# Kernel optimization log

Hardware: AMD Instinct MI355X
Metric: run time of the kernel (lower is better)

## Reference

```python
import jax, jax.numpy as jnp
import numpy as np

N, E, IN_DIM, HID, HEADS, LAT = 50000, 800000, 128, 32, 4, 32


def _gat_params(key, fin, heads, cout):
    k1, k2, k3 = jax.random.split(key, 3)
    s = 1.0 / np.sqrt(fin)
    W = jax.random.uniform(k1, (fin, heads * cout), minval=-s, maxval=s, dtype=jnp.float32)
    a_src = jax.random.normal(k2, (heads, cout), dtype=jnp.float32) * 0.1
    a_dst = jax.random.normal(k3, (heads, cout), dtype=jnp.float32) * 0.1
    b = jnp.zeros((heads * cout,), dtype=jnp.float32)
    return W, a_src, a_dst, b


def setup_inputs() -> dict:
    key = jax.random.key(0)
    ks = jax.random.split(key, 8)
    x = jax.random.normal(ks[0], (N, IN_DIM), dtype=jnp.float32)
    edge_index = jax.random.randint(ks[1], (2, E), 0, N, dtype=jnp.int64)
    W1, a1s, a1d, b1 = _gat_params(ks[2], IN_DIM, HEADS, HID)
    W2, a2s, a2d, b2 = _gat_params(ks[3], HID * HEADS, HEADS, HID)
    Wl, als, ald, bl = _gat_params(ks[4], HID * HEADS, 1, LAT)
    Wd, ads_, add_, bd = _gat_params(ks[5], LAT, 1, HID)
    sdec = 1.0 / np.sqrt(HID)
    Wdec = jax.random.uniform(ks[6], (HID, IN_DIM), minval=-sdec, maxval=sdec, dtype=jnp.float32)
    bdec = jnp.zeros((IN_DIM,), dtype=jnp.float32)
    return {"x": x, "edge_index": edge_index,
            "W1": W1, "a1s": a1s, "a1d": a1d, "b1": b1,
            "W2": W2, "a2s": a2s, "a2d": a2d, "b2": b2,
            "Wl": Wl, "als": als, "ald": ald, "bl": bl,
            "Wd": Wd, "ads": ads_, "add": add_, "bd": bd,
            "Wdec": Wdec, "bdec": bdec}


def gat_conv(x, src, dst, W, a_s, a_d, b, n, concat=True):
    """PyG-style GATConv (eval mode, self-loops already in src/dst)."""
    H, C = a_s.shape
    h = (x @ W).reshape(n, H, C)                      # [N,H,C]
    alpha_src = jnp.sum(h * a_s, axis=-1)             # [N,H]
    alpha_dst = jnp.sum(h * a_d, axis=-1)             # [N,H]
    e = jax.nn.leaky_relu(alpha_src[src] + alpha_dst[dst], 0.2)  # [E,H]
    m = jax.ops.segment_max(e, dst, num_segments=n)
    m = jnp.where(jnp.isfinite(m), m, 0.0)
    ex = jnp.exp(e - m[dst])
    denom = jax.ops.segment_sum(ex, dst, num_segments=n)
    coef = ex / (denom[dst] + 1e-16)                  # [E,H]
    out = jax.ops.segment_sum(coef[:, :, None] * h[src], dst, num_segments=n)  # [N,H,C]
    out = out.reshape(n, H * C) if concat else out.mean(axis=1)
    return out + b


def reference(x, edge_index, W1, a1s, a1d, b1, W2, a2s, a2d, b2,
              Wl, als, ald, bl, Wd, ads, add, bd, Wdec, bdec):
    n = x.shape[0]
    # add self-loops (PyG GATConv default)
    loops = jnp.arange(n, dtype=edge_index.dtype)
    src = jnp.concatenate([edge_index[0], loops])
    dst = jnp.concatenate([edge_index[1], loops])
    lrelu = lambda v: jax.nn.leaky_relu(v, 0.01)
    x1 = lrelu(gat_conv(x, src, dst, W1, a1s, a1d, b1, n))
    x2 = lrelu(gat_conv(x1, src, dst, W2, a2s, a2d, b2, n))
    z = gat_conv(x2, src, dst, Wl, als, ald, bl, n)
    xr = lrelu(gat_conv(z, src, dst, Wd, ads, add, bd, n))
    reconstructed = xr @ Wdec + bdec + x
    return reconstructed, z
```

## Files before the change

### kernel.cpp

```cpp
#include <hip/hip_runtime.h>
#include <math.h>

#define CAP 64

typedef __attribute__((ext_vector_type(8))) short short8;
typedef __attribute__((ext_vector_type(4))) float f32x4;

__device__ __forceinline__ float lrelu02(float v) { return v > 0.f ? v : 0.2f * v; }
__device__ __forceinline__ float lrelu01(float v) { return v > 0.f ? v : 0.01f * v; }

__device__ __forceinline__ float bfl(unsigned u) { return __uint_as_float(u << 16); }
__device__ __forceinline__ float bfh(unsigned u) { return __uint_as_float(u & 0xffff0000u); }
__device__ __forceinline__ unsigned short f2bf(float f) {
  unsigned u = __float_as_uint(f);
  return (unsigned short)((u + 0x7fffu + ((u >> 16) & 1u)) >> 16);
}
__device__ __forceinline__ unsigned pk2bf(float lo, float hi) {
  return (unsigned)f2bf(lo) | ((unsigned)f2bf(hi) << 16);
}

__global__ __launch_bounds__(256) void prep_k(const int* __restrict__ ei, int* __restrict__ deg,
                                              unsigned short* __restrict__ cols, int E, int nr, int Nn,
                                              const float* __restrict__ W1, const float* __restrict__ W2,
                                              const float* __restrict__ Wl,
                                              unsigned short* __restrict__ t1, unsigned short* __restrict__ t2,
                                              unsigned short* __restrict__ tl) {
  if (blockIdx.x < 2048) {
    const int r = blockIdx.x & 7;
    const int c = blockIdx.x >> 3;
    const unsigned lo = (unsigned)(r * nr);
    const unsigned hi = (unsigned)min(Nn, (r + 1) * nr);
    const int chunk = (E + 255) >> 8;
    const int e0 = c * chunk;
    const int e1 = min(E, e0 + chunk);
    for (int e = e0 + (int)threadIdx.x; e < e1; e += 256) {
      unsigned d = (unsigned)ei[E + e];
      if (d >= lo && d < hi) {
        int s = ei[e];
        int pos = atomicAdd(&deg[d], 1);
        if (pos < CAP) cols[(size_t)d * CAP + pos] = (unsigned short)s;
      }
    }
  } else {
    int b = blockIdx.x - 2048, tid = threadIdx.x;
    const float* src; unsigned short* dst; int K, NC, base;
    if (b < 64)       { src = W1; dst = t1; K = 128; NC = 128; base = 0; }
    else if (b < 128) { src = W2; dst = t2; K = 128; NC = 128; base = 64; }
    else              { src = Wl; dst = tl; K = 128; NC = 32;  base = 128; }
    int e = (b - base) * 256 + tid;
    if (e < K * NC) {
      int k = e / NC, c2 = e - k * NC;
      dst[c2 * K + k] = f2bf(src[e]);
    }
  }
}

template<int K, int NC, bool ALPHA, bool IN32>
__global__ __launch_bounds__(256) void gemm_mfma(const void* __restrict__ Av,
                                                 const unsigned short* __restrict__ Wt,
                                                 unsigned short* __restrict__ Cb,
                                                 const float* __restrict__ a_s, const float* __restrict__ a_d,
                                                 float* __restrict__ asrc, float* __restrict__ adst, int M) {
  constexpr int BM = (NC == 128) ? 64 : 128;
  constexpr int NKS = K / 32;
  constexpr int RS = (NC == 128) ? 4 : 2;
  constexpr int SWZ = 7;
  constexpr int CH = BM * K / 2048;
  __shared__ unsigned short At[BM * K];
  const int tid = threadIdx.x;
  const int wid = tid >> 6, lane = tid & 63;
  const int g = lane >> 4, l15 = lane & 15;
  const int row0 = blockIdx.x * BM;

  short8 wf[NKS][2];
  const int cglob0 = ((NC == 128) ? 32 * wid : 0) + l15;
#pragma unroll
  for (int ks = 0; ks < NKS; ++ks)
#pragma unroll
    for (int cf = 0; cf < 2; ++cf)
      wf[ks][cf] = *(const short8*)(Wt + (size_t)(cglob0 + 16 * cf) * K + ks * 32 + g * 8);

  uint4 ra[CH];
  if constexpr (IN32) {
    const float* Af = (const float*)Av;
#pragma unroll
    for (int c = 0; c < CH; ++c) {
      int ch = c * 256 + tid;
      int row = ch * 8 / K;
      int col = ch * 8 - row * K;
      float4 lo = {0.f, 0.f, 0.f, 0.f}, hi = {0.f, 0.f, 0.f, 0.f};
      if (row0 + row < M) {
        lo = *(const float4*)(Af + (size_t)(row0 + row) * K + col);
        hi = *(const float4*)(Af + (size_t)(row0 + row) * K + col + 4);
      }
      ra[c] = make_uint4(pk2bf(lo.x, lo.y), pk2bf(lo.z, lo.w), pk2bf(hi.x, hi.y), pk2bf(hi.z, hi.w));
    }
  } else {
    const unsigned short* Ab = (const unsigned short*)Av;
#pragma unroll
    for (int c = 0; c < CH; ++c) {
      int ch = c * 256 + tid;
      int row = ch * 8 / K;
      ra[c] = (row0 + row < M) ? *(const uint4*)(Ab + (size_t)row0 * K + ch * 8)
                               : make_uint4(0u, 0u, 0u, 0u);
    }
  }
#pragma unroll
  for (int c = 0; c < CH; ++c) {
    int ch = c * 256 + tid;
    int row = ch * 8 / K;
    int off = ch * 16 - row * (2 * K);
    *(uint4*)((char*)At + row * (2 * K) + (off ^ ((row & SWZ) << 4))) = ra[c];
  }
  __syncthreads();

  f32x4 acc[RS][2];
#pragma unroll
  for (int r = 0; r < RS; ++r)
#pragma unroll
    for (int cf = 0; cf < 2; ++cf) acc[r][cf] = (f32x4){0.f, 0.f, 0.f, 0.f};

  const int rwave = (NC == 128) ? 0 : 32 * wid;
#pragma unroll
  for (int ks = 0; ks < NKS; ++ks) {
#pragma unroll
    for (int r = 0; r < RS; ++r) {
      int row = rwave + 16 * r + l15;
      int off = ks * 64 + g * 16;
      short8 af = *(const short8*)((const char*)At + row * (2 * K) + (off ^ ((row & SWZ) << 4)));
#pragma unroll
      for (int cf = 0; cf < 2; ++cf)
        acc[r][cf] = __builtin_amdgcn_mfma_f32_16x16x32_bf16(wf[ks][cf], af, acc[r][cf], 0, 0, 0);
    }
  }

#pragma unroll
  for (int r = 0; r < RS; ++r) {
    const int row = row0 + rwave + 16 * r + l15;
    const bool ok = row < M;
#pragma unroll
    for (int cf = 0; cf < 2; ++cf) {
      const int colbase = ((NC == 128) ? 32 * wid : 0) + 16 * cf + 4 * g;
      if (ok) {
        ushort4 o;
        o.x = f2bf(acc[r][cf][0]); o.y = f2bf(acc[r][cf][1]);
        o.z = f2bf(acc[r][cf][2]); o.w = f2bf(acc[r][cf][3]);
        *(ushort4*)(Cb + (size_t)row * NC + colbase) = o;
      }
    }
    if constexpr (ALPHA) {
      constexpr int H = NC / 32;
      const int head = (NC == 128) ? wid : 0;
      float ps = 0.f, pd = 0.f;
#pragma unroll
      for (int cf = 0; cf < 2; ++cf) {
        float4 sa = *(const float4*)(a_s + head * 32 + 16 * cf + 4 * g);
        float4 da = *(const float4*)(a_d + head * 32 + 16 * cf + 4 * g);
        ps += acc[r][cf][0] * sa.x + acc[r][cf][1] * sa.y + acc[r][cf][2] * sa.z + acc[r][cf][3] * sa.w;
        pd += acc[r][cf][0] * da.x + acc[r][cf][1] * da.y + acc[r][cf][2] * da.z + acc[r][cf][3] * da.w;
      }
      ps += __shfl_xor(ps, 16, 64); pd += __shfl_xor(pd, 16, 64);
      ps += __shfl_xor(ps, 32, 64); pd += __shfl_xor(pd, 32, 64);
      if (g == 0 && ok) {
        asrc[(size_t)row * H + head] = ps;
        adst[(size_t)row * H + head] = pd;
      }
    }
  }
}

template<int ACT>
__global__ __launch_bounds__(256) void agg128_k(const unsigned short* __restrict__ Hb,
                                                const float* __restrict__ asrc,
                                                const float* __restrict__ adst,
                                                const int* __restrict__ deg,
                                                const unsigned short* __restrict__ cols,
                                                const float* __restrict__ bias,
                                                unsigned short* __restrict__ Y, int Nn) {
  __shared__ float wl[4][256];
  __shared__ int sl[4][64];
  const int wid = threadIdx.x >> 6, lane = threadIdx.x & 63;
  const int node = blockIdx.x * 4 + wid;
  if (node >= Nn) return;
  const int eidx = lane >> 2, h4 = lane & 3;
  const float adr = adst[node * 4 + h4];
  const float asr = asrc[node * 4 + h4];
  int cnt = deg[node];
  cnt = cnt > CAP ? CAP : cnt;
  const unsigned short* __restrict__ cl = cols + (size_t)node * CAP;
  float dn = 0.f;
  for (int c0 = 0; c0 < cnt; c0 += 16) {
    int e = c0 + eidx;
    bool valid = e < cnt;
    int s = valid ? (int)cl[e] : 0;
    float w = valid ? __expf(lrelu02(asrc[s * 4 + h4] + adr)) : 0.f;
    wl[wid][e * 4 + h4] = w;
    if (h4 == 0) sl[wid][e] = s * 16;
    dn += w;
  }
  dn += __shfl_xor(dn, 4, 64);
  dn += __shfl_xor(dn, 8, 64);
  dn += __shfl_xor(dn, 16, 64);
  dn += __shfl_xor(dn, 32, 64);
  float wself = __expf(lrelu02(asr + adr));
  dn += wself;
  float inv = 1.f / (dn + 1e-16f);
  float wsinv = wself * inv;
  for (int j = lane; j < cnt * 4; j += 64) wl[wid][j] *= inv;
  float wns = __shfl(wsinv, (lane & 15) >> 2, 64);
  __builtin_amdgcn_wave_barrier();

  const uint4* __restrict__ HB = (const uint4*)Hb;
  const int sub = lane >> 4;
  const int c8 = lane & 15;
  const int h = c8 >> 2;
  float a0 = 0.f, a1 = 0.f, a2 = 0.f, a3 = 0.f, a4 = 0.f, a5 = 0.f, a6 = 0.f, a7 = 0.f;
  float p0 = 0.f, p1 = 0.f, p2 = 0.f, p3 = 0.f, p4 = 0.f, p5 = 0.f, p6 = 0.f, p7 = 0.f;
  int i = sub;
  for (; i + 4 < cnt; i += 8) {
    int o0 = sl[wid][i];
    int o1 = sl[wid][i + 4];
    float w0 = wl[wid][i * 4 + h];
    float w1 = wl[wid][(i + 4) * 4 + h];
    uint4 u0 = HB[o0 + c8];
    uint4 u1 = HB[o1 + c8];
    a0 += w0 * bfl(u0.x); a1 += w0 * bfh(u0.x); a2 += w0 * bfl(u0.y); a3 += w0 * bfh(u0.y);
    a4 += w0 * bfl(u0.z); a5 += w0 * bfh(u0.z); a6 += w0 * bfl(u0.w); a7 += w0 * bfh(u0.w);
    p0 += w1 * bfl(u1.x); p1 += w1 * bfh(u1.x); p2 += w1 * bfl(u1.y); p3 += w1 * bfh(u1.y);
    p4 += w1 * bfl(u1.z); p5 += w1 * bfh(u1.z); p6 += w1 * bfl(u1.w); p7 += w1 * bfh(u1.w);
  }
  for (; i < cnt; i += 4) {
    int o0 = sl[wid][i];
    float w0 = wl[wid][i * 4 + h];
    uint4 u0 = HB[o0 + c8];
    a0 += w0 * bfl(u0.x); a1 += w0 * bfh(u0.x); a2 += w0 * bfl(u0.y); a3 += w0 * bfh(u0.y);
    a4 += w0 * bfl(u0.z); a5 += w0 * bfh(u0.z); a6 += w0 * bfl(u0.w); a7 += w0 * bfh(u0.w);
  }
  a0 += p0; a1 += p1; a2 += p2; a3 += p3; a4 += p4; a5 += p5; a6 += p6; a7 += p7;
#pragma unroll
  for (int off = 16; off <= 32; off <<= 1) {
    a0 += __shfl_xor(a0, off, 64); a1 += __shfl_xor(a1, off, 64);
    a2 += __shfl_xor(a2, off, 64); a3 += __shfl_xor(a3, off, 64);
    a4 += __shfl_xor(a4, off, 64); a5 += __shfl_xor(a5, off, 64);
    a6 += __shfl_xor(a6, off, 64); a7 += __shfl_xor(a7, off, 64);
  }
  if (lane < 16) {
    uint4 us = HB[node * 16 + c8];
    float4 b0 = *(const float4*)(bias + c8 * 8);
    float4 b1 = *(const float4*)(bias + c8 * 8 + 4);
    float o0 = a0 + wns * bfl(us.x) + b0.x;
    float o1 = a1 + wns * bfh(us.x) + b0.y;
    float o2 = a2 + wns * bfl(us.y) + b0.z;
    float o3 = a3 + wns * bfh(us.y) + b0.w;
    float o4 = a4 + wns * bfl(us.z) + b1.x;
    float o5 = a5 + wns * bfh(us.z) + b1.y;
    float o6 = a6 + wns * bfl(us.w) + b1.z;
    float o7 = a7 + wns * bfh(us.w) + b1.w;
    if (ACT == 1) {
      o0 = lrelu01(o0); o1 = lrelu01(o1); o2 = lrelu01(o2); o3 = lrelu01(o3);
      o4 = lrelu01(o4); o5 = lrelu01(o5); o6 = lrelu01(o6); o7 = lrelu01(o7);
    }
    ((uint4*)Y)[(size_t)node * 16 + c8] =
        make_uint4(pk2bf(o0, o1), pk2bf(o2, o3), pk2bf(o4, o5), pk2bf(o6, o7));
  }
}

template<int ACT>
__device__ __forceinline__ float4 agg32_core(const unsigned short* __restrict__ Hb,
                                             const float* __restrict__ asrc, const float* __restrict__ adst,
                                             const int* __restrict__ deg,
                                             const unsigned short* __restrict__ cols,
                                             const float* __restrict__ bias,
                                             float (*wl)[64], int (*sl)[64],
                                             int wid, int lane, int node) {
  const float adr = adst[node], asr = asrc[node];
  int cnt = deg[node];
  cnt = cnt > CAP ? CAP : cnt;
  const unsigned short* __restrict__ cl = cols + (size_t)node * CAP;
  int s = (lane < cnt) ? (int)cl[lane] : 0;
  float w = (lane < cnt) ? __expf(lrelu02(asrc[s] + adr)) : 0.f;
  float dn = w;
#pragma unroll
  for (int off = 32; off >= 1; off >>= 1) dn += __shfl_xor(dn, off, 64);
  float ws = __expf(lrelu02(asr + adr));
  dn += ws;
  float inv = 1.f / (dn + 1e-16f);
  wl[wid][lane] = w * inv;
  sl[wid][lane] = s * 8;
  __builtin_amdgcn_wave_barrier();

  const uint2* __restrict__ HB = (const uint2*)Hb;
  const int sub = lane >> 3;
  const int c = lane & 7;
  float a0 = 0.f, a1 = 0.f, a2 = 0.f, a3 = 0.f;
  float p0 = 0.f, p1 = 0.f, p2 = 0.f, p3 = 0.f;
  int i = sub;
  for (; i + 8 < cnt; i += 16) {
    int o0 = sl[wid][i];
    int o1 = sl[wid][i + 8];
    float w0 = wl[wid][i];
    float w1 = wl[wid][i + 8];
    uint2 u0 = HB[o0 + c];
    uint2 u1 = HB[o1 + c];
    a0 += w0 * bfl(u0.x); a1 += w0 * bfh(u0.x); a2 += w0 * bfl(u0.y); a3 += w0 * bfh(u0.y);
    p0 += w1 * bfl(u1.x); p1 += w1 * bfh(u1.x); p2 += w1 * bfl(u1.y); p3 += w1 * bfh(u1.y);
  }
  for (; i < cnt; i += 8) {
    int o0 = sl[wid][i];
    float w0 = wl[wid][i];
    uint2 u0 = HB[o0 + c];
    a0 += w0 * bfl(u0.x); a1 += w0 * bfh(u0.x); a2 += w0 * bfl(u0.y); a3 += w0 * bfh(u0.y);
  }
  a0 += p0; a1 += p1; a2 += p2; a3 += p3;
#pragma unroll
  for (int off = 8; off <= 32; off <<= 1) {
    a0 += __shfl_xor(a0, off, 64); a1 += __shfl_xor(a1, off, 64);
    a2 += __shfl_xor(a2, off, 64); a3 += __shfl_xor(a3, off, 64);
  }
  float4 out = make_float4(0.f, 0.f, 0.f, 0.f);
  if (lane < 8) {
    uint2 us = HB[node * 8 + c];
    float wns = ws * inv;
    float4 bb = ((const float4*)bias)[c];
    out.x = a0 + wns * bfl(us.x) + bb.x;
    out.y = a1 + wns * bfh(us.x) + bb.y;
    out.z = a2 + wns * bfl(us.y) + bb.z;
    out.w = a3 + wns * bfh(us.y) + bb.w;
    if (ACT == 1) { out.x = lrelu01(out.x); out.y = lrelu01(out.y); out.z = lrelu01(out.z); out.w = lrelu01(out.w); }
  }
  return out;
}

__global__ __launch_bounds__(256) void agg32_l3_k(const unsigned short* __restrict__ Hb,
                                                  const float* __restrict__ asrc, const float* __restrict__ adst,
                                                  const int* __restrict__ deg,
                                                  const unsigned short* __restrict__ cols,
                                                  const float* __restrict__ bl,
                                                  const float* __restrict__ Wd,
                                                  const float* __restrict__ ads, const float* __restrict__ add_,
                                                  float* __restrict__ zout, unsigned short* __restrict__ H4,
                                                  float* __restrict__ asrcB, float* __restrict__ adstB, int Nn) {
  __shared__ float Wd_l[32 * 32];
  __shared__ float wl[4][64];
  __shared__ int sl[4][64];
  __shared__ float zb[4][32];
  {
    int t = threadIdx.x * 4;
    *(float4*)&Wd_l[t] = *(const float4*)(Wd + t);
  }
  __syncthreads();
  const int wid = threadIdx.x >> 6, lane = threadIdx.x & 63;
  const int node = blockIdx.x * 4 + wid;
  if (node >= Nn) return;

  float4 z = agg32_core<0>(Hb, asrc, adst, deg, cols, bl, wl, sl, wid, lane, node);
  const int c = lane & 7;
  if (lane < 8) {
    ((float4*)zout)[(size_t)node * 8 + c] = z;
    *(float4*)&zb[wid][c * 4] = z;
  }
  __builtin_amdgcn_wave_barrier();

  float h4 = 0.f;
  const int j = lane & 31;
#pragma unroll 8
  for (int k = 0; k < 32; ++k) h4 += zb[wid][k] * Wd_l[k * 32 + j];
  float ps = 0.f, pd = 0.f;
  if (lane < 32) {
    H4[(size_t)node * 32 + j] = f2bf(h4);
    ps = h4 * ads[j];
    pd = h4 * add_[j];
  }
#pragma unroll
  for (int off = 1; off <= 16; off <<= 1) { ps += __shfl_xor(ps, off, 64); pd += __shfl_xor(pd, off, 64); }
  if (lane == 0) {
    asrcB[node] = ps;
    adstB[node] = pd;
  }
}

__global__ __launch_bounds__(256) void agg32_l4_k(const unsigned short* __restrict__ Hb,
                                                  const float* __restrict__ asrc, const float* __restrict__ adst,
                                                  const int* __restrict__ deg,
                                                  const unsigned short* __restrict__ cols,
                                                  const float* __restrict__ bd,
                                                  const float* __restrict__ Wdec,
                                                  const float* __restrict__ bdec,
                                                  const float* __restrict__ x,
                                                  float* __restrict__ rec, int Nn) {
  __shared__ float Wdec_l[32 * 128];
  __shared__ float wl[4][64];
  __shared__ int sl[4][64];
  __shared__ float xb[4][32];
  {
    int t = threadIdx.x * 16;
#pragma unroll
    for (int q = 0; q < 4; ++q)
      *(float4*)&Wdec_l[t + q * 4] = *(const float4*)(Wdec + t + q * 4);
  }
  __syncthreads();
  const int wid = threadIdx.x >> 6, lane = threadIdx.x & 63;
  const int node = blockIdx.x * 4 + wid;
  if (node >= Nn) return;

  float4 xr = agg32_core<1>(Hb, asrc, adst, deg, cols, bd, wl, sl, wid, lane, node);
  const int c = lane & 7;
  if (lane < 8) *(float4*)&xb[wid][c * 4] = xr;
  __builtin_amdgcn_wave_barrier();

  float r0 = 0.f, r1 = 0.f;
#pragma unroll 8
  for (int k = 0; k < 32; ++k) {
    float xv = xb[wid][k];
    r0 += xv * Wdec_l[k * 128 + lane];
    r1 += xv * Wdec_l[k * 128 + lane + 64];
  }
  r0 += bdec[lane] + x[(size_t)node * 128 + lane];
  r1 += bdec[lane + 64] + x[(size_t)node * 128 + lane + 64];
  rec[(size_t)node * 128 + lane] = r0;
  rec[(size_t)node * 128 + lane + 64] = r1;
}

extern "C" void kernel_launch(void* const* d_in, const int* in_sizes, int n_in,
                              void* d_out, int out_size, void* d_ws, size_t ws_size,
                              hipStream_t stream) {
  const float* x = (const float*)d_in[0];
  const int* ei = (const int*)d_in[1];
  const float* W1 = (const float*)d_in[2];
  const float* a1s = (const float*)d_in[3];
  const float* a1d = (const float*)d_in[4];
  const float* b1 = (const float*)d_in[5];
  const float* W2 = (const float*)d_in[6];
  const float* a2s = (const float*)d_in[7];
  const float* a2d = (const float*)d_in[8];
  const float* b2 = (const float*)d_in[9];
  const float* Wl = (const float*)d_in[10];
  const float* als = (const float*)d_in[11];
  const float* ald = (const float*)d_in[12];
  const float* bl = (const float*)d_in[13];
  const float* Wd = (const float*)d_in[14];
  const float* ads = (const float*)d_in[15];
  const float* add_ = (const float*)d_in[16];
  const float* bd = (const float*)d_in[17];
  const float* Wdec = (const float*)d_in[18];
  const float* bdec = (const float*)d_in[19];

  const int N = in_sizes[0] / 128;
  const int E = in_sizes[1] / 2;
  const int nr = (N + 7) / 8;

  char* ws = (char*)d_ws;
  auto alloc = [&](size_t bytes) {
    char* p = ws;
    ws += (bytes + 255) & ~(size_t)255;
    return p;
  };
  unsigned short* cols = (unsigned short*)alloc((size_t)N * CAP * 2);
  int* deg = (int*)alloc((size_t)N * 4);
  unsigned short* hb16 = (unsigned short*)alloc((size_t)N * 128 * 2);
  float* asrc = (float*)alloc((size_t)N * 4 * 4);
  float* adst = (float*)alloc((size_t)N * 4 * 4);
  float* asrcB = (float*)alloc((size_t)N * 4);
  float* adstB = (float*)alloc((size_t)N * 4);
  unsigned short* x12 = (unsigned short*)alloc((size_t)N * 128 * 2);
  unsigned short* hb2 = (unsigned short*)alloc((size_t)N * 32 * 2);
  unsigned short* W1t = (unsigned short*)alloc(128 * 128 * 2);
  unsigned short* W2t = (unsigned short*)alloc(128 * 128 * 2);
  unsigned short* Wlt = (unsigned short*)alloc(128 * 32 * 2);

  float* rec = (float*)d_out;
  float* zout = (float*)d_out + (size_t)N * 128;

  hipMemsetAsync(deg, 0, (size_t)N * 4, stream);
  prep_k<<<2192, 256, 0, stream>>>(ei, deg, cols, E, nr, N, W1, W2, Wl, W1t, W2t, Wlt);

  const int gG128 = (N + 63) / 64;
  const int gG32 = (N + 127) / 128;
  const int gAg = (N + 3) / 4;

  gemm_mfma<128, 128, true, true><<<gG128, 256, 0, stream>>>(
      x, W1t, hb16, a1s, a1d, asrc, adst, N);
  agg128_k<1><<<gAg, 256, 0, stream>>>(hb16, asrc, adst, deg, cols, b1, x12, N);

  gemm_mfma<128, 128, true, false><<<gG128, 256, 0, stream>>>(
      x12, W2t, hb16, a2s, a2d, asrc, adst, N);
  agg128_k<1><<<gAg, 256, 0, stream>>>(hb16, asrc, adst, deg, cols, b2, x12, N);

  gemm_mfma<128, 32, true, false><<<gG32, 256, 0, stream>>>(
      x12, Wlt, hb16, als, ald, asrc, adst, N);
  agg32_l3_k<<<gAg, 256, 0, stream>>>(hb16, asrc, adst, deg, cols, bl, Wd, ads, add_,
                                      zout, hb2, asrcB, adstB, N);
  agg32_l4_k<<<gAg, 256, 0, stream>>>(hb2, asrcB, adstB, deg, cols, bd, Wdec, bdec, x, rec, N);
}
```

Measured before the change: 332.5 us.

## Move decoder GEMM out of layer-4 aggregation into bf16 MFMA kernel

```diff
diff --git a/kernel.cpp b/kernel.cpp
--- a/kernel.cpp
+++ b/kernel.cpp
@@ -55,16 +55,18 @@
   }
 }
 
-template<int K, int NC, bool ALPHA, bool IN32>
+template<int K, int NC, bool OUT16, bool ALPHA, bool RB, bool IN32>
 __global__ __launch_bounds__(256) void gemm_mfma(const void* __restrict__ Av,
                                                  const unsigned short* __restrict__ Wt,
-                                                 unsigned short* __restrict__ Cb,
+                                                 const float* __restrict__ bias,
+                                                 const float* __restrict__ resid,
+                                                 void* __restrict__ Cv,
                                                  const float* __restrict__ a_s, const float* __restrict__ a_d,
                                                  float* __restrict__ asrc, float* __restrict__ adst, int M) {
   constexpr int BM = (NC == 128) ? 64 : 128;
   constexpr int NKS = K / 32;
   constexpr int RS = (NC == 128) ? 4 : 2;
-  constexpr int SWZ = 7;
+  constexpr int SWZ = (K == 128) ? 7 : 3;
   constexpr int CH = BM * K / 2048;
   __shared__ unsigned short At[BM * K];
   const int tid = threadIdx.x;
@@ -141,11 +143,26 @@
 #pragma unroll
     for (int cf = 0; cf < 2; ++cf) {
       const int colbase = ((NC == 128) ? 32 * wid : 0) + 16 * cf + 4 * g;
-      if (ok) {
-        ushort4 o;
-        o.x = f2bf(acc[r][cf][0]); o.y = f2bf(acc[r][cf][1]);
-        o.z = f2bf(acc[r][cf][2]); o.w = f2bf(acc[r][cf][3]);
-        *(ushort4*)(Cb + (size_t)row * NC + colbase) = o;
+      if constexpr (OUT16) {
+        if (ok) {
+          unsigned short* Cb = (unsigned short*)Cv;
+          ushort4 o;
+          o.x = f2bf(acc[r][cf][0]); o.y = f2bf(acc[r][cf][1]);
+          o.z = f2bf(acc[r][cf][2]); o.w = f2bf(acc[r][cf][3]);
+          *(ushort4*)(Cb + (size_t)row * NC + colbase) = o;
+        }
+      } else if constexpr (RB) {
+        if (ok) {
+          float* C = (float*)Cv;
+          float4 bi = *(const float4*)(bias + colbase);
+          float4 rv = *(const float4*)(resid + (size_t)row * NC + colbase);
+          float4 o;
+          o.x = acc[r][cf][0] + bi.x + rv.x;
+          o.y = acc[r][cf][1] + bi.y + rv.y;
+          o.z = acc[r][cf][2] + bi.z + rv.z;
+          o.w = acc[r][cf][3] + bi.w + rv.w;
+          *(float4*)(C + (size_t)row * NC + colbase) = o;
+        }
       }
     }
     if constexpr (ALPHA) {
@@ -384,41 +401,17 @@
                                                   const int* __restrict__ deg,
                                                   const unsigned short* __restrict__ cols,
                                                   const float* __restrict__ bd,
-                                                  const float* __restrict__ Wdec,
-                                                  const float* __restrict__ bdec,
-                                                  const float* __restrict__ x,
-                                                  float* __restrict__ rec, int Nn) {
-  __shared__ float Wdec_l[32 * 128];
+                                                  unsigned short* __restrict__ Y, int Nn) {
   __shared__ float wl[4][64];
   __shared__ int sl[4][64];
-  __shared__ float xb[4][32];
-  {
-    int t = threadIdx.x * 16;
-#pragma unroll
-    for (int q = 0; q < 4; ++q)
-      *(float4*)&Wdec_l[t + q * 4] = *(const float4*)(Wdec + t + q * 4);
-  }
-  __syncthreads();
   const int wid = threadIdx.x >> 6, lane = threadIdx.x & 63;
   const int node = blockIdx.x * 4 + wid;
   if (node >= Nn) return;
-
   float4 xr = agg32_core<1>(Hb, asrc, adst, deg, cols, bd, wl, sl, wid, lane, node);
   const int c = lane & 7;
-  if (lane < 8) *(float4*)&xb[wid][c * 4] = xr;
-  __builtin_amdgcn_wave_barrier();
-
-  float r0 = 0.f, r1 = 0.f;
-#pragma unroll 8
-  for (int k = 0; k < 32; ++k) {
-    float xv = xb[wid][k];
-    r0 += xv * Wdec_l[k * 128 + lane];
-    r1 += xv * Wdec_l[k * 128 + lane + 64];
-  }
-  r0 += bdec[lane] + x[(size_t)node * 128 + lane];
-  r1 += bdec[lane + 64] + x[(size_t)node * 128 + lane + 64];
-  rec[(size_t)node * 128 + lane] = r0;
-  rec[(size_t)node * 128 + lane + 64] = r1;
+  if (lane < 8) {
+    ((uint2*)Y)[(size_t)node * 8 + c] = make_uint2(pk2bf(xr.x, xr.y), pk2bf(xr.z, xr.w));
+  }
 }
 
 extern "C" void kernel_launch(void* const* d_in, const int* in_sizes, int n_in,
@@ -464,9 +457,11 @@
   float* adstB = (float*)alloc((size_t)N * 4);
   unsigned short* x12 = (unsigned short*)alloc((size_t)N * 128 * 2);
   unsigned short* hb2 = (unsigned short*)alloc((size_t)N * 32 * 2);
+  unsigned short* xr16 = (unsigned short*)alloc((size_t)N * 32 * 2);
   unsigned short* W1t = (unsigned short*)alloc(128 * 128 * 2);
   unsigned short* W2t = (unsigned short*)alloc(128 * 128 * 2);
   unsigned short* Wlt = (unsigned short*)alloc(128 * 32 * 2);
+  unsigned short* Wdect = (unsigned short*)alloc(32 * 128 * 2);
 
   float* rec = (float*)d_out;
   float* zout = (float*)d_out + (size_t)N * 128;
@@ -478,17 +473,32 @@
   const int gG32 = (N + 127) / 128;
   const int gAg = (N + 3) / 4;
 
-  gemm_mfma<128, 128, true, true><<<gG128, 256, 0, stream>>>(
-      x, W1t, hb16, a1s, a1d, asrc, adst, N);
+  {
+    struct L { static __global__ void k(const float* __restrict__ src, unsigned short* __restrict__ dst) {
+      int e = blockIdx.x * 256 + threadIdx.x;
+      if (e < 32 * 128) {
+        int k = e / 128, c = e - k * 128;
+        dst[c * 32 + k] = f2bf(src[e]);
+      }
+    } };
+    hipLaunchKernelGGL(L::k, dim3(16), dim3(256), 0, stream, Wdec, Wdect);
+  }
+
+  gemm_mfma<128, 128, true, true, false, true><<<gG128, 256, 0, stream>>>(
+      x, W1t, nullptr, nullptr, hb16, a1s, a1d, asrc, adst, N);
   agg128_k<1><<<gAg, 256, 0, stream>>>(hb16, asrc, adst, deg, cols, b1, x12, N);
 
-  gemm_mfma<128, 128, true, false><<<gG128, 256, 0, stream>>>(
-      x12, W2t, hb16, a2s, a2d, asrc, adst, N);
+  gemm_mfma<128, 128, true, true, false, false><<<gG128, 256, 0, stream>>>(
+      x12, W2t, nullptr, nullptr, hb16, a2s, a2d, asrc, adst, N);
   agg128_k<1><<<gAg, 256, 0, stream>>>(hb16, asrc, adst, deg, cols, b2, x12, N);
 
-  gemm_mfma<128, 32, true, false><<<gG32, 256, 0, stream>>>(
-      x12, Wlt, hb16, als, ald, asrc, adst, N);
+  gemm_mfma<128, 32, true, true, false, false><<<gG32, 256, 0, stream>>>(
+      x12, Wlt, nullptr, nullptr, hb16, als, ald, asrc, adst, N);
   agg32_l3_k<<<gAg, 256, 0, stream>>>(hb16, asrc, adst, deg, cols, bl, Wd, ads, add_,
                                       zout, hb2, asrcB, adstB, N);
-  agg32_l4_k<<<gAg, 256, 0, stream>>>(hb2, asrcB, adstB, deg, cols, bd, Wdec, bdec, x, rec, N);
-}
+
+  agg32_l4_k<<<gAg, 256, 0, stream>>>(hb2, asrcB, adstB, deg, cols, bd, xr16, N);
+
+  gemm_mfma<32, 128, false, false, true, false><<<gG128, 256, 0, stream>>>(
+      xr16, Wdect, bdec, x, rec, nullptr, nullptr, nullptr, nullptr, N);
+}
```

New measurement: 328.1 us. Within noise of the previous version (-1.3%).
